# Performance work log

Measured on AMD Instinct MI355X. Metric: run time of the kernel, lower is better.

## Reference

```python
import jax, jax.numpy as jnp
import numpy as np
import math

N_NODES = 1048576   # total rows of x
N_SEG = 8192        # number of hyperedges (segments)
D_IN = 128
D_H = 64            # hidden_dim == embed_dim of the MHA


def setup_inputs() -> dict:
    key = jax.random.key(0)
    ks = jax.random.split(key, 12)
    x = jax.random.normal(ks[0], (N_NODES, D_IN), dtype=jnp.float32)
    # offset: sorted, with fixed endpoints 0 and N_NODES (torch.split semantics)
    cuts = jnp.sort(jax.random.randint(ks[1], (N_SEG - 1,), 0, N_NODES, dtype=jnp.int32))
    offset = jnp.concatenate([jnp.zeros((1,), jnp.int32), cuts,
                              jnp.full((1,), N_NODES, jnp.int32)])
    s1 = 1.0 / math.sqrt(D_IN)
    s2 = 1.0 / math.sqrt(D_H)
    W1 = jax.random.normal(ks[2], (D_H, D_IN), jnp.float32) * s1
    b1 = jax.random.normal(ks[3], (D_H,), jnp.float32) * s1
    W2 = jax.random.normal(ks[4], (D_H, D_H), jnp.float32) * s2
    b2 = jax.random.normal(ks[5], (D_H,), jnp.float32) * s2
    in_proj_w = jax.random.normal(ks[6], (3 * D_H, D_H), jnp.float32) * s2
    in_proj_b = jax.random.normal(ks[7], (3 * D_H,), jnp.float32) * s2
    out_w = jax.random.normal(ks[8], (D_H, D_H), jnp.float32) * s2
    out_b = jax.random.normal(ks[9], (D_H,), jnp.float32) * s2
    return {"x": x, "offset": offset, "W1": W1, "b1": b1, "W2": W2, "b2": b2,
            "in_proj_w": in_proj_w, "in_proj_b": in_proj_b,
            "out_w": out_w, "out_b": out_b}


def reference(x, offset, W1, b1, W2, b2, in_proj_w, in_proj_b, out_w, out_b):
    n = x.shape[0]
    n_seg = offset.shape[0] - 1
    # phi MLP: Linear->ReLU->Linear->ReLU
    h = jax.nn.relu(x @ W1.T + b1)
    h = jax.nn.relu(h @ W2.T + b2)                      # [N, 64]
    # ragged segment-sum pooling (torch.split + per-slice sum, fused)
    seg_ids = jnp.searchsorted(offset, jnp.arange(n, dtype=offset.dtype),
                               side='right') - 1
    tokens = jax.ops.segment_sum(h, seg_ids, num_segments=n_seg)  # [S, 64]
    # MultiheadAttention with batch_first=False: input is [L=1, batch=S, E=64],
    # so each token attends over a length-1 sequence.
    Wq, Wk, Wv = jnp.split(in_proj_w, 3, axis=0)
    bq, bk, bv = jnp.split(in_proj_b, 3, axis=0)
    t = tokens[:, None, :]                               # [S, 1, E]
    q = t @ Wq.T + bq
    k = t @ Wk.T + bk
    v = t @ Wv.T + bv
    scale = 1.0 / math.sqrt(t.shape[-1])
    scores = jnp.einsum('sqe,ske->sqk', q, k) * scale    # [S, 1, 1]
    attn = jax.nn.softmax(scores, axis=-1)               # trivially ones
    ctx = jnp.einsum('sqk,ske->sqe', attn, v)[:, 0]      # [S, 64]
    return ctx @ out_w.T + out_b
```

## Files before the change

kernel.cpp:

```cpp
#include <hip/hip_runtime.h>
#include <math.h>

#define NNODES 1048576
#define NSEG   8192
#define DIN    128
#define DH     64

typedef __bf16 bf16x8 __attribute__((ext_vector_type(8)));
typedef __bf16 bf16x4 __attribute__((ext_vector_type(4)));
typedef float  f32x4  __attribute__((ext_vector_type(4)));

__global__ void seg_fill_kernel(const int* __restrict__ offset, int* __restrict__ seg_id,
                                float* __restrict__ tokens) {
    int s = blockIdx.x;
    tokens[s * DH + (int)threadIdx.x] = 0.f;
    int start = offset[s], end = offset[s + 1];
    for (int i = start + (int)threadIdx.x; i < end; i += (int)blockDim.x) seg_id[i] = s;
}

__global__ void fold_kernel(const float* __restrict__ in_proj_w, const float* __restrict__ in_proj_b,
                            const float* __restrict__ out_w, const float* __restrict__ out_b,
                            float* __restrict__ Mt, float* __restrict__ bfold) {
    int t = blockIdx.x * blockDim.x + threadIdx.x;
    int i = t >> 6, j = t & 63;
    const float* Wv = in_proj_w + 2 * DH * DH;
    float sum = 0.f;
#pragma unroll 8
    for (int k = 0; k < DH; ++k) sum += out_w[i * DH + k] * Wv[k * DH + j];
    Mt[j * DH + i] = sum;
    if (t < DH) {
        const float* bv = in_proj_b + 2 * DH;
        float s2 = out_b[t];
#pragma unroll 8
        for (int k = 0; k < DH; ++k) s2 += out_w[t * DH + k] * bv[k];
        bfold[t] = s2;
    }
}

__device__ __forceinline__ void stage16x8(const char* src_lane, float* lds_base) {
#pragma unroll
    for (int i = 0; i < 8; ++i)
        __builtin_amdgcn_global_load_lds(
            (const __attribute__((address_space(1))) void*)(src_lane + i * 64),
            (__attribute__((address_space(3))) void*)((char*)lds_base + i * 1024),
            16, 0, 0);
}

__launch_bounds__(256, 2)
__global__ void mlp_seg_kernel(const float* __restrict__ x, const int* __restrict__ seg_id,
                               const float* __restrict__ W1, const float* __restrict__ b1,
                               const float* __restrict__ W2, const float* __restrict__ b2,
                               float* __restrict__ tokens) {
    const int tid  = threadIdx.x;
    const int w    = tid >> 6;
    const int lane = tid & 63;
    const int quad = lane >> 4;
    const int col  = lane & 15;

    __shared__ __align__(16) float  xstage[4][2][2048];
    __shared__ __align__(16) __bf16 h1w[4][16][72];

    bf16x8 w1f[4][4];
#pragma unroll
    for (int nt = 0; nt < 4; ++nt)
#pragma unroll
        for (int kt = 0; kt < 4; ++kt) {
            const float* wp = W1 + (nt * 16 + col) * DIN + kt * 32 + quad * 8;
#pragma unroll
            for (int j = 0; j < 8; ++j) w1f[nt][kt][j] = (__bf16)wp[j];
        }
    bf16x8 w2f[4][2];
#pragma unroll
    for (int nt = 0; nt < 4; ++nt)
#pragma unroll
        for (int kt = 0; kt < 2; ++kt) {
            const float* wp = W2 + (nt * 16 + col) * DH + kt * 32 + quad * 8;
#pragma unroll
            for (int j = 0; j < 8; ++j) w2f[nt][kt][j] = (__bf16)wp[j];
        }
    float4 b1q[4];
    float  b2v[4];
#pragma unroll
    for (int nt = 0; nt < 4; ++nt) {
        b1q[nt] = *(const float4*)(b1 + nt * 16 + quad * 4);
        b2v[nt] = b2[nt * 16 + col];
    }

    const int nb0 = blockIdx.x * 256 + w * 64;
    const int seg_all = seg_id[nb0 + lane];

    const char* src0 = (const char*)(x + (size_t)(nb0 + col) * DIN + quad * 4);

    float* sbuf0 = &xstage[w][0][0];
    float* sbuf1 = &xstage[w][1][0];
    stage16x8(src0,        sbuf0);
    stage16x8(src0 + 8192, sbuf1);

#pragma unroll
    for (int t = 0; t < 4; ++t) {
        if (t < 3) asm volatile("s_waitcnt vmcnt(8)" ::: "memory");
        else       asm volatile("s_waitcnt vmcnt(0)" ::: "memory");
        __builtin_amdgcn_sched_barrier(0);

        const float4* sb = (const float4*)((t & 1) ? sbuf1 : sbuf0);

        bf16x8 a[4];
#pragma unroll
        for (int kt = 0; kt < 4; ++kt) {
            float4 u  = sb[(kt * 8 + quad * 2) * 16 + col];
            float4 v2 = sb[(kt * 8 + quad * 2 + 1) * 16 + col];
            a[kt][0] = (__bf16)u.x;  a[kt][1] = (__bf16)u.y;
            a[kt][2] = (__bf16)u.z;  a[kt][3] = (__bf16)u.w;
            a[kt][4] = (__bf16)v2.x; a[kt][5] = (__bf16)v2.y;
            a[kt][6] = (__bf16)v2.z; a[kt][7] = (__bf16)v2.w;
        }

        f32x4 acc1[4];
#pragma unroll
        for (int nt = 0; nt < 4; ++nt) acc1[nt] = (f32x4){0.f, 0.f, 0.f, 0.f};
#pragma unroll
        for (int kt = 0; kt < 4; ++kt)
#pragma unroll
            for (int nt = 0; nt < 4; ++nt)
                acc1[nt] = __builtin_amdgcn_mfma_f32_16x16x32_bf16(w1f[nt][kt], a[kt], acc1[nt], 0, 0, 0);

#pragma unroll
        for (int nt = 0; nt < 4; ++nt) {
            bf16x4 hw;
#pragma unroll
            for (int r = 0; r < 4; ++r)
                hw[r] = (__bf16)fmaxf(acc1[nt][r] + ((const float*)&b1q[nt])[r], 0.f);
            *(bf16x4*)&h1w[w][col][nt * 16 + quad * 4] = hw;
        }

        bf16x8 a2[2];
#pragma unroll
        for (int kt = 0; kt < 2; ++kt)
            a2[kt] = *(const bf16x8*)&h1w[w][col][kt * 32 + quad * 8];

        f32x4 acc2[4];
#pragma unroll
        for (int nt = 0; nt < 4; ++nt) acc2[nt] = (f32x4){0.f, 0.f, 0.f, 0.f};
#pragma unroll
        for (int kt = 0; kt < 2; ++kt)
#pragma unroll
            for (int nt = 0; nt < 4; ++nt)
                acc2[nt] = __builtin_amdgcn_mfma_f32_16x16x32_bf16(a2[kt], w2f[nt][kt], acc2[nt], 0, 0, 0);

        float hv[4][4];
#pragma unroll
        for (int nt = 0; nt < 4; ++nt)
#pragma unroll
            for (int r = 0; r < 4; ++r)
                hv[nt][r] = fmaxf(acc2[nt][r] + b2v[nt], 0.f);

        int s0 = __shfl(seg_all, t * 16);
        int s1 = __shfl(seg_all, t * 16 + 15);
        if (s0 == s1) {
            float p[4];
#pragma unroll
            for (int nt = 0; nt < 4; ++nt) {
                p[nt] = hv[nt][0] + hv[nt][1] + hv[nt][2] + hv[nt][3];
                p[nt] += __shfl_xor(p[nt], 16);
                p[nt] += __shfl_xor(p[nt], 32);
            }
            float val = (quad == 0) ? p[0] : (quad == 1) ? p[1] : (quad == 2) ? p[2] : p[3];
            atomicAdd(&tokens[s0 * DH + quad * 16 + col], val);
        } else {
            int segs[4];
#pragma unroll
            for (int r = 0; r < 4; ++r) segs[r] = __shfl(seg_all, t * 16 + quad * 4 + r);
#pragma unroll
            for (int nt = 0; nt < 4; ++nt)
#pragma unroll
                for (int r = 0; r < 4; ++r)
                    atomicAdd(&tokens[segs[r] * DH + nt * 16 + col], hv[nt][r]);
        }

        __builtin_amdgcn_sched_barrier(0);
        if (t == 0) stage16x8(src0 + 2 * 8192, sbuf0);
        if (t == 1) stage16x8(src0 + 3 * 8192, sbuf1);
        __builtin_amdgcn_sched_barrier(0);
    }
}

__global__ void out_kernel(const float* __restrict__ tokens, const float* __restrict__ Mt,
                           const float* __restrict__ bfold, float* __restrict__ out) {
    __shared__ float mt[DH * DH];
    __shared__ float bf[DH];
    for (int i = threadIdx.x; i < DH * DH; i += 256) mt[i] = Mt[i];
    if (threadIdx.x < DH) bf[threadIdx.x] = bfold[threadIdx.x];
    __syncthreads();
    int sl = threadIdx.x >> 6;
    int d  = threadIdx.x & 63;
    int s  = blockIdx.x * 4 + sl;
    const float* trow = tokens + s * DH;
    float sum = bf[d];
#pragma unroll 16
    for (int k = 0; k < DH; ++k) sum += trow[k] * mt[k * DH + d];
    out[s * DH + d] = sum;
}

extern "C" void kernel_launch(void* const* d_in, const int* in_sizes, int n_in,
                              void* d_out, int out_size, void* d_ws, size_t ws_size,
                              hipStream_t stream) {
    const float* x         = (const float*)d_in[0];
    const int*   offset    = (const int*)d_in[1];
    const float* W1        = (const float*)d_in[2];
    const float* b1        = (const float*)d_in[3];
    const float* W2        = (const float*)d_in[4];
    const float* b2        = (const float*)d_in[5];
    const float* in_proj_w = (const float*)d_in[6];
    const float* in_proj_b = (const float*)d_in[7];
    const float* out_w     = (const float*)d_in[8];
    const float* out_b     = (const float*)d_in[9];
    float* out = (float*)d_out;

    char* ws = (char*)d_ws;
    float* tokens = (float*)ws;
    int*   seg_id = (int*)(ws + (size_t)NSEG * DH * 4);
    float* Mt     = (float*)(ws + (size_t)NSEG * DH * 4 + (size_t)NNODES * 4);
    float* bfold  = Mt + DH * DH;

    seg_fill_kernel<<<NSEG, 64, 0, stream>>>(offset, seg_id, tokens);
    fold_kernel<<<16, 256, 0, stream>>>(in_proj_w, in_proj_b, out_w, out_b, Mt, bfold);
    mlp_seg_kernel<<<NNODES / 256, 256, 0, stream>>>(x, seg_id, W1, b1, W2, b2, tokens);
    out_kernel<<<NSEG / 4, 256, 0, stream>>>(tokens, Mt, bfold, out);
}
```

Measured before the change: 775.4 us.

## Compute segment ids by in-kernel binary search and double rows per block

Drops the seg_fill kernel and its 4 MB seg_id array. Each wave now finds its rows' segment ids with a binary search over offset plus a short linear scan. Token zeroing moves into the fold kernel. The MLP kernel now handles 512 rows per block (128 per wave), running 8 double-buffered stages, which amortises the per-block weight-fragment loads over more rows. The cost is extra dependent global loads for the search at kernel start and half as many blocks in flight.

```diff
diff --git a/kernel.cpp b/kernel.cpp
--- a/kernel.cpp
+++ b/kernel.cpp
@@ -10,24 +10,20 @@
 typedef __bf16 bf16x4 __attribute__((ext_vector_type(4)));
 typedef float  f32x4  __attribute__((ext_vector_type(4)));
 
-__global__ void seg_fill_kernel(const int* __restrict__ offset, int* __restrict__ seg_id,
-                                float* __restrict__ tokens) {
-    int s = blockIdx.x;
-    tokens[s * DH + (int)threadIdx.x] = 0.f;
-    int start = offset[s], end = offset[s + 1];
-    for (int i = start + (int)threadIdx.x; i < end; i += (int)blockDim.x) seg_id[i] = s;
-}
-
 __global__ void fold_kernel(const float* __restrict__ in_proj_w, const float* __restrict__ in_proj_b,
                             const float* __restrict__ out_w, const float* __restrict__ out_b,
-                            float* __restrict__ Mt, float* __restrict__ bfold) {
-    int t = blockIdx.x * blockDim.x + threadIdx.x;
-    int i = t >> 6, j = t & 63;
-    const float* Wv = in_proj_w + 2 * DH * DH;
-    float sum = 0.f;
+                            float* __restrict__ Mt, float* __restrict__ bfold,
+                            float* __restrict__ tokens) {
+    int t = blockIdx.x * 256 + (int)threadIdx.x;
+    ((float4*)tokens)[t] = make_float4(0.f, 0.f, 0.f, 0.f);
+    if (t < DH * DH) {
+        int i = t >> 6, j = t & 63;
+        const float* Wv = in_proj_w + 2 * DH * DH;
+        float sum = 0.f;
 #pragma unroll 8
-    for (int k = 0; k < DH; ++k) sum += out_w[i * DH + k] * Wv[k * DH + j];
-    Mt[j * DH + i] = sum;
+        for (int k = 0; k < DH; ++k) sum += out_w[i * DH + k] * Wv[k * DH + j];
+        Mt[j * DH + i] = sum;
+    }
     if (t < DH) {
         const float* bv = in_proj_b + 2 * DH;
         float s2 = out_b[t];
@@ -47,7 +43,7 @@
 }
 
 __launch_bounds__(256, 2)
-__global__ void mlp_seg_kernel(const float* __restrict__ x, const int* __restrict__ seg_id,
+__global__ void mlp_seg_kernel(const float* __restrict__ x, const int* __restrict__ offset,
                                const float* __restrict__ W1, const float* __restrict__ b1,
                                const float* __restrict__ W2, const float* __restrict__ b2,
                                float* __restrict__ tokens) {
@@ -60,6 +56,25 @@
     __shared__ __align__(16) float  xstage[4][2][2048];
     __shared__ __align__(16) __bf16 h1w[4][16][72];
 
+    const int nb0 = blockIdx.x * 512 + w * 128;
+
+    int seg_g[2];
+    {
+        int i0 = nb0 + lane;
+        int lo = 0, hi = NSEG;
+#pragma unroll 1
+        for (int it = 0; it < 13; ++it) {
+            int mid = (lo + hi) >> 1;
+            bool ge = (offset[mid] <= i0);
+            lo = ge ? mid : lo;
+            hi = ge ? hi : mid;
+        }
+        seg_g[0] = lo;
+        int i1 = i0 + 64, s = lo;
+        while (offset[s + 1] <= i1) ++s;
+        seg_g[1] = s;
+    }
+
     bf16x8 w1f[4][4];
 #pragma unroll
     for (int nt = 0; nt < 4; ++nt)
@@ -85,9 +100,6 @@
         b1q[nt] = *(const float4*)(b1 + nt * 16 + quad * 4);
         b2v[nt] = b2[nt * 16 + col];
     }
-
-    const int nb0 = blockIdx.x * 256 + w * 64;
-    const int seg_all = seg_id[nb0 + lane];
 
     const char* src0 = (const char*)(x + (size_t)(nb0 + col) * DIN + quad * 4);
 
@@ -97,8 +109,8 @@
     stage16x8(src0 + 8192, sbuf1);
 
 #pragma unroll
-    for (int t = 0; t < 4; ++t) {
-        if (t < 3) asm volatile("s_waitcnt vmcnt(8)" ::: "memory");
+    for (int t = 0; t < 8; ++t) {
+        if (t < 7) asm volatile("s_waitcnt vmcnt(8)" ::: "memory");
         else       asm volatile("s_waitcnt vmcnt(0)" ::: "memory");
         __builtin_amdgcn_sched_barrier(0);
 
@@ -154,8 +166,9 @@
             for (int r = 0; r < 4; ++r)
                 hv[nt][r] = fmaxf(acc2[nt][r] + b2v[nt], 0.f);
 
-        int s0 = __shfl(seg_all, t * 16);
-        int s1 = __shfl(seg_all, t * 16 + 15);
+        const int sg = seg_g[t >> 2];
+        int s0 = __shfl(sg, (t & 3) * 16);
+        int s1 = __shfl(sg, (t & 3) * 16 + 15);
         if (s0 == s1) {
             float p[4];
 #pragma unroll
@@ -169,7 +182,7 @@
         } else {
             int segs[4];
 #pragma unroll
-            for (int r = 0; r < 4; ++r) segs[r] = __shfl(seg_all, t * 16 + quad * 4 + r);
+            for (int r = 0; r < 4; ++r) segs[r] = __shfl(sg, (t & 3) * 16 + quad * 4 + r);
 #pragma unroll
             for (int nt = 0; nt < 4; ++nt)
 #pragma unroll
@@ -178,8 +191,7 @@
         }
 
         __builtin_amdgcn_sched_barrier(0);
-        if (t == 0) stage16x8(src0 + 2 * 8192, sbuf0);
-        if (t == 1) stage16x8(src0 + 3 * 8192, sbuf1);
+        if (t < 6) stage16x8(src0 + (size_t)(t + 2) * 8192, (t & 1) ? sbuf1 : sbuf0);
         __builtin_amdgcn_sched_barrier(0);
     }
 }
@@ -218,12 +230,10 @@
 
     char* ws = (char*)d_ws;
     float* tokens = (float*)ws;
-    int*   seg_id = (int*)(ws + (size_t)NSEG * DH * 4);
-    float* Mt     = (float*)(ws + (size_t)NSEG * DH * 4 + (size_t)NNODES * 4);
+    float* Mt     = (float*)(ws + (size_t)NSEG * DH * 4);
     float* bfold  = Mt + DH * DH;
 
-    seg_fill_kernel<<<NSEG, 64, 0, stream>>>(offset, seg_id, tokens);
-    fold_kernel<<<16, 256, 0, stream>>>(in_proj_w, in_proj_b, out_w, out_b, Mt, bfold);
-    mlp_seg_kernel<<<NNODES / 256, 256, 0, stream>>>(x, seg_id, W1, b1, W2, b2, tokens);
+    fold_kernel<<<512, 256, 0, stream>>>(in_proj_w, in_proj_b, out_w, out_b, Mt, bfold, tokens);
+    mlp_seg_kernel<<<NNODES / 512, 256, 0, stream>>>(x, offset, W1, b1, W2, b2, tokens);
     out_kernel<<<NSEG / 4, 256, 0, stream>>>(tokens, Mt, bfold, out);
 }
```

New measurement: 776.6 us. Within noise of the previous version (+0.1%).
